# Performance work log

Hardware: AMD Instinct MI355X
Metric: run time of the kernel (lower is better)

Reference implementation:

```python
import jax, jax.numpy as jnp
import numpy as np

B, T, N_EMBD = 4, 2048, 1024
NUM_EXPERTS, TOP_K = 8, 2
N_CITIES = 4
LIN = N_EMBD + 32 + N_EMBD // 4 + N_EMBD // 4 + N_EMBD // 8 + N_EMBD // 8  # 1824


def setup_inputs() -> dict:
    key = jax.random.key(0)
    ks = jax.random.split(key, 12)
    s = 0.02  # init std as in _init_weights
    return {
        "x": jax.random.normal(ks[0], (B, T, N_EMBD), jnp.float32),
        "delta_t_info": jax.random.normal(ks[1], (B, T, N_EMBD // 4), jnp.float32),
        "delta_dis_info": jax.random.normal(ks[2], (B, T, N_EMBD // 4), jnp.float32),
        "delta_rg_info": jax.random.normal(ks[3], (B, T, N_EMBD // 8), jnp.float32),
        "delta_entropy_info": jax.random.normal(ks[4], (B, T, N_EMBD // 8), jnp.float32),
        "city_embeddings": jax.random.normal(ks[5], (N_CITIES, 32), jnp.float32),
        "Wg": jax.random.normal(ks[6], (LIN, NUM_EXPERTS), jnp.float32) * s,
        "bg": jnp.zeros((NUM_EXPERTS,), jnp.float32),
        "W1": jax.random.normal(ks[7], (NUM_EXPERTS, N_EMBD, 4 * N_EMBD), jnp.float32) * s,
        "b1": jnp.zeros((NUM_EXPERTS, 4 * N_EMBD), jnp.float32),
        "W2": jax.random.normal(ks[8], (NUM_EXPERTS, 4 * N_EMBD, N_EMBD), jnp.float32) * s,
        "b2": jnp.zeros((NUM_EXPERTS, N_EMBD), jnp.float32),
        "city_index": 1,
    }


def _moe(x, dt, dd, drg, de, city_embeddings, Wg, bg, W1, b1, W2, b2, city_index):
    b, t, _ = x.shape
    city = jnp.broadcast_to(city_embeddings[city_index], (b, t, 32))
    feats = jnp.concatenate([x, city, dt, dd, drg, de], axis=-1)  # [B,T,LIN]
    logits = jnp.einsum("btl,le->bte", feats, Wg) + bg            # eval mode: no noise
    gate1 = jax.nn.softmax(logits, axis=-1)
    _, topi = jax.lax.top_k(logits, TOP_K)                        # [B,T,k]
    # mask of top-k experts per token; scatter(-inf elsewhere) + softmax
    mask = jax.nn.one_hot(topi, NUM_EXPERTS, dtype=jnp.float32).sum(axis=-2) > 0
    sparse_logits = jnp.where(mask, logits, -jnp.inf)
    gates = jax.nn.softmax(sparse_logits, axis=-1)                # zeros outside top-k
    out = jnp.zeros_like(x)
    for e in range(NUM_EXPERTS):  # fixed small expert set
        h = jax.nn.gelu(jnp.einsum("btc,ch->bth", x, W1[e]) + b1[e], approximate=True)
        y = jnp.einsum("bth,hc->btc", h, W2[e]) + b2[e]
        out = out + gates[..., e:e + 1] * y  # gate is exactly 0 for non-topk tokens
    return out, gate1


def reference(x, delta_t_info, delta_dis_info, delta_rg_info, delta_entropy_info,
              city_embeddings, Wg, bg, W1, b1, W2, b2, city_index):
    return _moe(x, delta_t_info, delta_dis_info, delta_rg_info, delta_entropy_info,
                city_embeddings, Wg, bg, W1, b1, W2, b2, city_index)
```

## Files before the change

kernel.cpp:

```cpp
#include <hip/hip_runtime.h>
#include <hip/hip_bf16.h>
#include <stdint.h>

#define NTOK 8192
#define DEMB 1024
#define HDIM 4096
#define NEXP 8
#define LINF 1824
#define MAXPAD 17280

typedef __attribute__((ext_vector_type(8))) __bf16 bf16x8;
typedef __attribute__((ext_vector_type(4))) __bf16 bf16x4v;
typedef __attribute__((ext_vector_type(4))) float f32x4;

__device__ __forceinline__ void gload_lds16(const void* g, void* l) {
  __builtin_amdgcn_global_load_lds(
      (const __attribute__((address_space(1))) void*)g,
      (__attribute__((address_space(3))) void*)l, 16, 0, 0);
}

__device__ __forceinline__ float dot4(float4 a, float4 b) {
  return a.x*b.x + a.y*b.y + a.z*b.z + a.w*b.w;
}

__global__ void __launch_bounds__(256) k_logits(
    const float* __restrict__ x, const float* __restrict__ dt,
    const float* __restrict__ dd, const float* __restrict__ drg,
    const float* __restrict__ de, const float* __restrict__ city,
    const float* __restrict__ Wg, const float* __restrict__ bg,
    const int* __restrict__ city_index,
    float* __restrict__ gate1, int* __restrict__ top_i, float2* __restrict__ top_g)
{
  __shared__ float WgT[NEXP * LINF];
  const int tid = threadIdx.x;
  const float4* Wg4 = (const float4*)Wg;
  for (int i = tid; i < LINF * NEXP / 4; i += 256) {
    float4 v = Wg4[i];
    int e0 = (i & 1) * 4, f = i >> 1;
    WgT[(e0+0)*LINF + f] = v.x; WgT[(e0+1)*LINF + f] = v.y;
    WgT[(e0+2)*LINF + f] = v.z; WgT[(e0+3)*LINF + f] = v.w;
  }
  __syncthreads();

  const int wave = tid >> 6, lane = tid & 63;
  const int ci = city_index[0];
  const float4* city4 = (const float4*)(city + ci*32);
  const float4 z4 = {0.f, 0.f, 0.f, 0.f};

  #pragma unroll
  for (int k = 0; k < 4; ++k) {
    const int t = blockIdx.x*16 + wave*4 + k;
    const float4* x4 = (const float4*)x + (size_t)t*256;
    float4 xv0 = x4[lane], xv1 = x4[64+lane], xv2 = x4[128+lane], xv3 = x4[192+lane];
    float4 cv = (lane < 8) ? city4[lane] : z4;
    float4 tv = ((const float4*)dt)[(size_t)t*64 + lane];
    float4 dv = ((const float4*)dd)[(size_t)t*64 + lane];
    float4 rv = z4, ev = z4;
    if (lane < 32) {
      rv = ((const float4*)drg)[(size_t)t*32 + lane];
      ev = ((const float4*)de )[(size_t)t*32 + lane];
    }
    float a[8];
    const int l8 = lane & 7, l32 = lane & 31;
    #pragma unroll
    for (int e = 0; e < 8; ++e) {
      const float4* W = (const float4*)(WgT + e*LINF);
      float s = dot4(xv0, W[lane]) + dot4(xv1, W[64+lane])
              + dot4(xv2, W[128+lane]) + dot4(xv3, W[192+lane]);
      s += dot4(cv, W[256 + l8]);
      s += dot4(tv, W[264 + lane]) + dot4(dv, W[328 + lane]);
      s += dot4(rv, W[392 + l32]) + dot4(ev, W[424 + l32]);
      a[e] = s;
    }
    #pragma unroll
    for (int off = 32; off > 0; off >>= 1)
      #pragma unroll
      for (int e = 0; e < 8; ++e) a[e] += __shfl_xor(a[e], off);

    float lg[8];
    #pragma unroll
    for (int e = 0; e < 8; ++e) lg[e] = a[e] + bg[e];
    float mx = lg[0];
    #pragma unroll
    for (int e = 1; e < 8; ++e) mx = fmaxf(mx, lg[e]);
    float ex[8]; float s = 0.f;
    #pragma unroll
    for (int e = 0; e < 8; ++e) { ex[e] = expf(lg[e] - mx); s += ex[e]; }
    int i1 = 0; float l1 = lg[0];
    #pragma unroll
    for (int e = 1; e < 8; ++e) if (lg[e] > l1) { l1 = lg[e]; i1 = e; }
    int i2 = -1; float l2 = -1e30f;
    #pragma unroll
    for (int e = 0; e < 8; ++e) if (e != i1 && lg[e] > l2) { l2 = lg[e]; i2 = e; }
    float e2 = expf(l2 - l1);

    if (lane == 0) {
      float inv = 1.f / s;
      float4 o0 = { ex[0]*inv, ex[1]*inv, ex[2]*inv, ex[3]*inv };
      float4 o1 = { ex[4]*inv, ex[5]*inv, ex[6]*inv, ex[7]*inv };
      float4* gp = (float4*)(gate1 + (size_t)t*8);
      gp[0] = o0; gp[1] = o1;
      top_i[t] = i1 | (i2 << 4);
      float2 g = { 1.f / (1.f + e2), e2 / (1.f + e2) };
      top_g[t] = g;
    }
  }
}

__global__ void __launch_bounds__(256) k_build(
    const int* __restrict__ top_i, const float2* __restrict__ top_g,
    int* __restrict__ counts, int* __restrict__ ex_tok, float* __restrict__ ex_gate,
    int2* __restrict__ ppos)
{
  __shared__ int lcnt[8], lbase[8];
  const int tid = threadIdx.x;
  if (tid < 8) lcnt[tid] = 0;
  __syncthreads();
  const int t = blockIdx.x*256 + tid;
  const int ti = top_i[t];
  const int i1 = ti & 15, i2 = ti >> 4;
  const float2 g = top_g[t];
  int p1 = atomicAdd(&lcnt[i1], 1);
  int p2 = atomicAdd(&lcnt[i2], 1);
  __syncthreads();
  if (tid < 8) lbase[tid] = atomicAdd(&counts[tid], lcnt[tid]);
  __syncthreads();
  int s1 = lbase[i1] + p1; ex_tok[i1*NTOK+s1] = t; ex_gate[i1*NTOK+s1] = g.x;
  int s2 = lbase[i2] + p2; ex_tok[i2*NTOK+s2] = t; ex_gate[i2*NTOK+s2] = g.y;
  int2 pp = { i1 | (s1 << 3), i2 | (s2 << 3) };
  ppos[t] = pp;
}

__global__ void k_finalize(const int* __restrict__ counts, int* __restrict__ seg) {
  if (threadIdx.x == 0 && blockIdx.x == 0) {
    int s = 0;
    for (int e = 0; e < 8; ++e) { seg[e] = s; s += (counts[e] + 127) & ~127; }
    seg[8] = s;
  }
}

__global__ void __launch_bounds__(256) k_conv_x(
    const float4* __restrict__ x, bf16x4v* __restrict__ xb, int n4)
{
  int step = gridDim.x * blockDim.x;
  for (int i = blockIdx.x*blockDim.x + threadIdx.x; i < n4; i += step) {
    float4 v = x[i];
    bf16x4v o;
    o[0] = (__bf16)v.x; o[1] = (__bf16)v.y; o[2] = (__bf16)v.z; o[3] = (__bf16)v.w;
    xb[i] = o;
  }
}

template<int RDIM, int CDIM>
__global__ void __launch_bounds__(256) k_tconv(
    const float* __restrict__ W, __bf16* __restrict__ WT)
{
  const int e  = blockIdx.z;
  const int c0 = blockIdx.x * 64, r0 = blockIdx.y * 64;
  __shared__ float tbuf[64][65];
  const float* src = W  + (size_t)e * RDIM * CDIM;
  __bf16*      dst = WT + (size_t)e * RDIM * CDIM;
  const int tx = threadIdx.x & 63, ty = threadIdx.x >> 6;
  #pragma unroll
  for (int rr = ty; rr < 64; rr += 4)
    tbuf[rr][tx] = src[(size_t)(r0+rr)*CDIM + c0 + tx];
  __syncthreads();
  #pragma unroll
  for (int cc = ty; cc < 64; cc += 4)
    dst[(size_t)(c0+cc)*RDIM + r0 + tx] = (__bf16)tbuf[tx][cc];
}

template<int KDIM, int NDIM, bool G1>
__global__ void __launch_bounds__(512, 2) k_moe_gemm(
    const __bf16* __restrict__ Abase, const __bf16* __restrict__ WT,
    const float* __restrict__ bias,
    const int* __restrict__ seg, const int* __restrict__ counts,
    const int* __restrict__ ex_tok,
    int chunk0, __bf16* __restrict__ dstbuf)
{
  constexpr int NT = KDIM / 64;
  constexpr int BUFB = 49152;

  const int nx = gridDim.x, ny = gridDim.y;
  const int nwg = nx * ny;
  int flat = blockIdx.x + nx * blockIdx.y;
  {
    int q = nwg >> 3, r = nwg & 7;
    int xcd = flat & 7, idx = flat >> 3;
    flat = (xcd < r ? xcd * (q + 1) : r * (q + 1) + (xcd - r) * q) + idx;
  }
  int bx, by;
  if (G1) { bx = flat % nx; by = flat / nx; }
  else    { by = flat % ny; bx = flat / ny; }

  const int segtot = seg[8];
  const int row0 = chunk0 + bx * 128;
  if (row0 >= segtot) return;
  int e = 0;
  #pragma unroll
  for (int qq = 1; qq < 8; ++qq) if (row0 >= seg[qq]) e = qq;
  const int cnt  = counts[e];
  const int sege = seg[e];
  const int n0 = by * 256;

  __shared__ __align__(16) char smem[3 * BUFB];

  const int tid = threadIdx.x;
  const int wid = tid >> 6, lane = tid & 63;
  const int wm = wid >> 2, wn = wid & 3;
  const int l15 = lane & 15, l4 = lane >> 4;
  const __bf16* Bsrc = WT + (size_t)e * NDIM * KDIM;

  const __bf16* asrc[2]; const __bf16* bsrc[4];
  #pragma unroll
  for (int i = 0; i < 2; ++i) {
    int g = i*512 + tid;
    int rr = g >> 3;
    int kb = (g & 7) ^ (rr & 7);
    int arow;
    if (G1) {
      int lr = row0 + rr - sege;
      arow = (lr < cnt) ? ex_tok[e*NTOK + lr] : 0;
    } else {
      arow = row0 + rr - chunk0;
    }
    asrc[i] = Abase + (size_t)arow * KDIM + kb*8;
  }
  #pragma unroll
  for (int i = 0; i < 4; ++i) {
    int g = i*512 + tid;
    int rr = g >> 3;
    int kb = (g & 7) ^ (rr & 7);
    bsrc[i] = Bsrc + (size_t)(n0 + rr) * KDIM + kb*8;
  }

  int aoff[2][4], boff[2][4];
  #pragma unroll
  for (int kk = 0; kk < 2; ++kk) {
    const int kblk = kk*4 + l4;
    const int xo = (kblk ^ (l15 & 7)) * 16;
    #pragma unroll
    for (int m = 0; m < 4; ++m)
      aoff[kk][m] = (wm*64 + m*16 + l15)*128 + xo;
    #pragma unroll
    for (int n = 0; n < 4; ++n)
      boff[kk][n] = 16384 + (wn*64 + n*16 + l15)*128 + xo;
  }

  float bv[4];
  #pragma unroll
  for (int n = 0; n < 4; ++n)
    bv[n] = bias[(size_t)e*NDIM + n0 + wn*64 + n*16 + l15];

  auto STAGE = [&](int t, int b) {
    char* base = smem + b*BUFB;
    #pragma unroll
    for (int i = 0; i < 2; ++i)
      gload_lds16(asrc[i] + t*64, base + (i*512 + tid)*16);
    #pragma unroll
    for (int i = 0; i < 4; ++i)
      gload_lds16(bsrc[i] + t*64, base + 16384 + (i*512 + tid)*16);
  };

  f32x4 acc[4][4] = {};

  STAGE(0, 0);
  STAGE(1, 1);
  asm volatile("s_waitcnt vmcnt(6)" ::: "memory");
  __builtin_amdgcn_s_barrier();
  __builtin_amdgcn_sched_barrier(0);

  int cur = 0;
  for (int t = 0; t < NT; ++t) {
    const char* cb = smem + cur*BUFB;
    if (t + 2 < NT) {
      int b2 = cur + 2; if (b2 >= 3) b2 -= 3;
      __builtin_amdgcn_sched_barrier(0);
      STAGE(t + 2, b2);
      __builtin_amdgcn_sched_barrier(0);
    }
    #pragma unroll
    for (int kk = 0; kk < 2; ++kk) {
      bf16x8 af[4], bfv[4];
      #pragma unroll
      for (int m = 0; m < 4; ++m) af[m]  = *(const bf16x8*)(cb + aoff[kk][m]);
      #pragma unroll
      for (int n = 0; n < 4; ++n) bfv[n] = *(const bf16x8*)(cb + boff[kk][n]);
      __builtin_amdgcn_s_setprio(1);
      #pragma unroll
      for (int m = 0; m < 4; ++m)
        #pragma unroll
        for (int n = 0; n < 4; ++n)
          acc[m][n] = __builtin_amdgcn_mfma_f32_16x16x32_bf16(af[m], bfv[n], acc[m][n], 0, 0, 0);
      __builtin_amdgcn_s_setprio(0);
    }
    __builtin_amdgcn_sched_barrier(0);
    asm volatile("s_waitcnt lgkmcnt(0)" ::: "memory");
    if (t + 2 < NT) asm volatile("s_waitcnt vmcnt(6)" ::: "memory");
    else            asm volatile("s_waitcnt vmcnt(0)" ::: "memory");
    __builtin_amdgcn_s_barrier();
    __builtin_amdgcn_sched_barrier(0);
    cur = (cur == 2) ? 0 : cur + 1;
  }

  __bf16* Cl = (__bf16*)smem;
  #pragma unroll
  for (int n = 0; n < 4; ++n) {
    #pragma unroll
    for (int m = 0; m < 4; ++m) {
      #pragma unroll
      for (int r2 = 0; r2 < 4; ++r2) {
        float v = acc[m][n][r2] + bv[n];
        if (G1) {
          float z = 2.302208f * (v + 0.044715f * v * v * v);
          v = v / (1.f + exp2f(-z));
        }
        Cl[(wm*64 + m*16 + l4*4 + r2)*256 + wn*64 + n*16 + l15] = (__bf16)v;
      }
    }
  }
  __syncthreads();
  const int drow0 = G1 ? (row0 - chunk0) : row0;
  #pragma unroll
  for (int it = 0; it < 8; ++it) {
    int idx2 = it*512 + tid;
    int rr = idx2 >> 5, c8 = (idx2 & 31) * 8;
    *(bf16x8*)(dstbuf + (size_t)(drow0 + rr)*NDIM + n0 + c8) =
        *(const bf16x8*)(Cl + rr*256 + c8);
  }
}

__global__ void __launch_bounds__(256) k_combine(
    const __bf16* __restrict__ pbuf, const int2* __restrict__ ppos,
    const float2* __restrict__ top_g, const int* __restrict__ seg,
    float* __restrict__ out)
{
  const int t = blockIdx.x;
  const int tid = threadIdx.x;
  const int2 pp = ppos[t];
  const float2 g = top_g[t];
  const int e1 = pp.x & 7, i1 = pp.x >> 3;
  const int e2 = pp.y & 7, i2 = pp.y >> 3;
  const __bf16* r1 = pbuf + (size_t)(seg[e1] + i1) * DEMB;
  const __bf16* r2 = pbuf + (size_t)(seg[e2] + i2) * DEMB;
  float* orow = out + (size_t)t * DEMB;
  const int c = tid * 4;
  bf16x4v a = *(const bf16x4v*)(r1 + c);
  bf16x4v b = *(const bf16x4v*)(r2 + c);
  float4 o;
  o.x = g.x*(float)a[0] + g.y*(float)b[0];
  o.y = g.x*(float)a[1] + g.y*(float)b[1];
  o.z = g.x*(float)a[2] + g.y*(float)b[2];
  o.w = g.x*(float)a[3] + g.y*(float)b[3];
  *(float4*)(orow + c) = o;
}

extern "C" void kernel_launch(void* const* d_in, const int* in_sizes, int n_in,
                              void* d_out, int out_size, void* d_ws, size_t ws_size,
                              hipStream_t stream)
{
  const float* x   = (const float*)d_in[0];
  const float* dt  = (const float*)d_in[1];
  const float* dd  = (const float*)d_in[2];
  const float* drg = (const float*)d_in[3];
  const float* de  = (const float*)d_in[4];
  const float* city= (const float*)d_in[5];
  const float* Wg  = (const float*)d_in[6];
  const float* bg  = (const float*)d_in[7];
  const float* W1  = (const float*)d_in[8];
  const float* b1  = (const float*)d_in[9];
  const float* W2  = (const float*)d_in[10];
  const float* b2  = (const float*)d_in[11];
  const int* city_index = (const int*)d_in[12];

  float* out   = (float*)d_out;
  float* gate1 = out + (size_t)NTOK * DEMB;

  char* p = (char*)d_ws;
  int*    counts  = (int*)p;      p += 256;
  int*    seg     = (int*)p;      p += 256;
  int*    top_i   = (int*)p;      p += (size_t)NTOK*4;
  float2* top_g   = (float2*)p;   p += (size_t)NTOK*8;
  int2*   ppos    = (int2*)p;     p += (size_t)NTOK*8;
  int*    ex_tok  = (int*)p;      p += (size_t)NTOK*NEXP*4;
  float*  ex_gate = (float*)p;    p += (size_t)NTOK*NEXP*4;
  __bf16* xb      = (__bf16*)p;   p += (size_t)NTOK*DEMB*2;
  __bf16* W1T     = (__bf16*)p;   p += (size_t)NEXP*DEMB*HDIM*2;
  __bf16* W2T     = (__bf16*)p;   p += (size_t)NEXP*DEMB*HDIM*2;
  __bf16* pbuf    = (__bf16*)p;   p += (size_t)MAXPAD*DEMB*2;
  __bf16* hbuf    = (__bf16*)p;

  size_t fixed = (size_t)(p - (char*)d_ws);
  int CH = MAXPAD;
  while (CH > 0 && fixed + (size_t)CH * HDIM * 2 > ws_size) CH -= 256;
  if (CH <= 0) return;
  int nch = (MAXPAD + CH - 1) / CH;

  (void)hipMemsetAsync(counts, 0, 64, stream);

  k_conv_x<<<2048, 256, 0, stream>>>((const float4*)x, (bf16x4v*)xb, NTOK*DEMB/4);
  k_tconv<DEMB, HDIM><<<dim3(HDIM/64, DEMB/64, NEXP), 256, 0, stream>>>(W1, W1T);
  k_tconv<HDIM, DEMB><<<dim3(DEMB/64, HDIM/64, NEXP), 256, 0, stream>>>(W2, W2T);

  k_logits<<<NTOK/16, 256, 0, stream>>>(x, dt, dd, drg, de, city, Wg, bg,
                                        city_index, gate1, top_i, top_g);
  k_build<<<NTOK/256, 256, 0, stream>>>(top_i, top_g, counts, ex_tok, ex_gate, ppos);
  k_finalize<<<1, 64, 0, stream>>>(counts, seg);

  for (int c = 0; c < nch; ++c) {
    k_moe_gemm<DEMB, HDIM, true><<<dim3(CH/128, HDIM/256), 512, 0, stream>>>(
        xb, W1T, b1, seg, counts, ex_tok, c*CH, hbuf);
    k_moe_gemm<HDIM, DEMB, false><<<dim3(CH/128, DEMB/256), 512, 0, stream>>>(
        hbuf, W2T, b2, seg, counts, ex_tok, c*CH, pbuf);
  }
  k_combine<<<NTOK, 256, 0, stream>>>(pbuf, ppos, top_g, seg, out);
}
```

Before: 589.2 us.

## Interleave prefetch loads with MFMA phases and vectorize weight transpose-convert

The GEMM main loop splits each K-tile into two phases. Each phase issues its LDS fragment reads together with half of the next-next-stage global-to-LDS loads, then runs its MFMAs, with extra workgroup barriers between phases. The goal is to spread memory issue across compute instead of bursting all stage loads up front. Separately, the weight transpose/convert kernel now uses float4 loads and 16-byte bf16x8 stores in place of scalar accesses. The extra barriers add synchronization cost and could stall waves.

```diff
diff --git a/kernel.cpp b/kernel.cpp
--- a/kernel.cpp
+++ b/kernel.cpp
@@ -157,17 +157,28 @@
 {
   const int e  = blockIdx.z;
   const int c0 = blockIdx.x * 64, r0 = blockIdx.y * 64;
-  __shared__ float tbuf[64][65];
-  const float* src = W  + (size_t)e * RDIM * CDIM;
-  __bf16*      dst = WT + (size_t)e * RDIM * CDIM;
-  const int tx = threadIdx.x & 63, ty = threadIdx.x >> 6;
-  #pragma unroll
-  for (int rr = ty; rr < 64; rr += 4)
-    tbuf[rr][tx] = src[(size_t)(r0+rr)*CDIM + c0 + tx];
-  __syncthreads();
-  #pragma unroll
-  for (int cc = ty; cc < 64; cc += 4)
-    dst[(size_t)(c0+cc)*RDIM + r0 + tx] = (__bf16)tbuf[tx][cc];
+  __shared__ float tb[64 * 65];
+  const float* src = W  + (size_t)e * RDIM * CDIM + (size_t)r0 * CDIM + c0;
+  __bf16*      dst = WT + (size_t)e * RDIM * CDIM + (size_t)c0 * RDIM + r0;
+  const int tx = threadIdx.x & 15, ty = threadIdx.x >> 4;
+  #pragma unroll
+  for (int i = 0; i < 4; ++i) {
+    int r = ty + i*16;
+    float4 v = *(const float4*)(src + (size_t)r*CDIM + tx*4);
+    tb[(tx*4+0)*65 + r] = v.x; tb[(tx*4+1)*65 + r] = v.y;
+    tb[(tx*4+2)*65 + r] = v.z; tb[(tx*4+3)*65 + r] = v.w;
+  }
+  __syncthreads();
+  const int seg = threadIdx.x & 7, dr8 = threadIdx.x >> 3;
+  #pragma unroll
+  for (int i = 0; i < 2; ++i) {
+    int d = dr8 + i*32;
+    const float* row = tb + d*65 + seg*8;
+    bf16x8 o;
+    #pragma unroll
+    for (int j = 0; j < 8; ++j) o[j] = (__bf16)row[j];
+    *(bf16x8*)(dst + (size_t)d*RDIM + seg*8) = o;
+  }
 }
 
 template<int KDIM, int NDIM, bool G1>
@@ -273,19 +284,23 @@
   int cur = 0;
   for (int t = 0; t < NT; ++t) {
     const char* cb = smem + cur*BUFB;
-    if (t + 2 < NT) {
-      int b2 = cur + 2; if (b2 >= 3) b2 -= 3;
+    int b2 = cur + 2; if (b2 >= 3) b2 -= 3;
+    char* sb = smem + b2*BUFB;
+    const bool dost = (t + 2 < NT);
+
+    {
+      bf16x8 af[4], bfv[4];
+      #pragma unroll
+      for (int m = 0; m < 4; ++m) af[m]  = *(const bf16x8*)(cb + aoff[0][m]);
+      #pragma unroll
+      for (int n = 0; n < 4; ++n) bfv[n] = *(const bf16x8*)(cb + boff[0][n]);
+      if (dost) {
+        gload_lds16(asrc[0] + (t+2)*64, sb + (0*512 + tid)*16);
+        gload_lds16(asrc[1] + (t+2)*64, sb + (1*512 + tid)*16);
+        gload_lds16(bsrc[0] + (t+2)*64, sb + 16384 + (0*512 + tid)*16);
+      }
       __builtin_amdgcn_sched_barrier(0);
-      STAGE(t + 2, b2);
-      __builtin_amdgcn_sched_barrier(0);
-    }
-    #pragma unroll
-    for (int kk = 0; kk < 2; ++kk) {
-      bf16x8 af[4], bfv[4];
-      #pragma unroll
-      for (int m = 0; m < 4; ++m) af[m]  = *(const bf16x8*)(cb + aoff[kk][m]);
-      #pragma unroll
-      for (int n = 0; n < 4; ++n) bfv[n] = *(const bf16x8*)(cb + boff[kk][n]);
+      __builtin_amdgcn_s_barrier();
       __builtin_amdgcn_s_setprio(1);
       #pragma unroll
       for (int m = 0; m < 4; ++m)
@@ -293,13 +308,36 @@
         for (int n = 0; n < 4; ++n)
           acc[m][n] = __builtin_amdgcn_mfma_f32_16x16x32_bf16(af[m], bfv[n], acc[m][n], 0, 0, 0);
       __builtin_amdgcn_s_setprio(0);
-    }
-    __builtin_amdgcn_sched_barrier(0);
-    asm volatile("s_waitcnt lgkmcnt(0)" ::: "memory");
-    if (t + 2 < NT) asm volatile("s_waitcnt vmcnt(6)" ::: "memory");
-    else            asm volatile("s_waitcnt vmcnt(0)" ::: "memory");
-    __builtin_amdgcn_s_barrier();
-    __builtin_amdgcn_sched_barrier(0);
+      __builtin_amdgcn_sched_barrier(0);
+      __builtin_amdgcn_s_barrier();
+    }
+    {
+      bf16x8 af[4], bfv[4];
+      #pragma unroll
+      for (int m = 0; m < 4; ++m) af[m]  = *(const bf16x8*)(cb + aoff[1][m]);
+      #pragma unroll
+      for (int n = 0; n < 4; ++n) bfv[n] = *(const bf16x8*)(cb + boff[1][n]);
+      if (dost) {
+        gload_lds16(bsrc[1] + (t+2)*64, sb + 16384 + (1*512 + tid)*16);
+        gload_lds16(bsrc[2] + (t+2)*64, sb + 16384 + (2*512 + tid)*16);
+        gload_lds16(bsrc[3] + (t+2)*64, sb + 16384 + (3*512 + tid)*16);
+      }
+      __builtin_amdgcn_sched_barrier(0);
+      __builtin_amdgcn_s_barrier();
+      __builtin_amdgcn_s_setprio(1);
+      #pragma unroll
+      for (int m = 0; m < 4; ++m)
+        #pragma unroll
+        for (int n = 0; n < 4; ++n)
+          acc[m][n] = __builtin_amdgcn_mfma_f32_16x16x32_bf16(af[m], bfv[n], acc[m][n], 0, 0, 0);
+      __builtin_amdgcn_s_setprio(0);
+      __builtin_amdgcn_sched_barrier(0);
+      asm volatile("s_waitcnt lgkmcnt(0)" ::: "memory");
+      if (dost) asm volatile("s_waitcnt vmcnt(6)" ::: "memory");
+      else      asm volatile("s_waitcnt vmcnt(0)" ::: "memory");
+      __builtin_amdgcn_s_barrier();
+      __builtin_amdgcn_sched_barrier(0);
+    }
     cur = (cur == 2) ? 0 : cur + 1;
   }
 
```

Result: faster. 549.2 us (-6.8%).
